# Performance work log

Hardware: AMD Instinct MI355X
Metric: run time of the kernel (lower is better)

## Reference

```python
import jax, jax.numpy as jnp
import numpy as np

B, L, D, ORDER, POS, HID, LMAX = 4, 4096, 1024, 2, 65, 64, 4096
K2 = (POS - 1) // 2

def _layernorm(x, w, b, eps=1e-5):
    m = jnp.mean(x, -1, keepdims=True)
    v = jnp.mean((x - m) ** 2, -1, keepdims=True)
    return (x - m) * jax.lax.rsqrt(v + eps) * w + b

def _fftconv(x, h, d):
    # torch: rfft(h, 2L, norm='forward') * rfft(x, 2L) -> irfft(.., norm='forward')
    # net scaling equals standard (unnormalized fwd / 1-over-n inverse) circular conv,
    # which is exactly jnp.fft default conventions.
    n = 2 * x.shape[-1]
    y = jnp.fft.irfft(jnp.fft.rfft(x, n=n) * jnp.fft.rfft(h, n=n), n=n)[..., : x.shape[-1]]
    return y + x * d

def setup_inputs() -> dict:
    key = jax.random.key(0)
    ks = jax.random.split(key, 12)
    s = 0.05
    # PositionalEncoding buffers/params (deterministic init, as in torch __init__)
    t = np.linspace(0, 1, LMAX, dtype=np.float64)[:, None]
    t_pos = np.arange(LMAX, dtype=np.float64)[:, None]
    k = np.arange(K2, dtype=np.float64)[None, :]
    z = np.exp(1j * 2 * np.pi * k * t_pos / LMAX)
    pos_z = np.concatenate([t, z.real, z.imag], axis=-1).astype(np.float32)  # (LMAX, POS)
    pos_t = t.reshape(1, 1, LMAX).astype(np.float32)
    # ExponentialDecayWindow alphas (deterministic init)
    max_decay = np.log(0.01) / 0.3
    min_decay = np.log(0.01) / 1.5
    alphas = np.linspace(min_decay, max_decay, D).reshape(1, D, 1).astype(np.float32)
    H3 = (ORDER + 1) * D
    return dict(
        u=jax.random.normal(ks[0], (B, L, D), jnp.float32),
        norm1_w=jnp.ones((D,), jnp.float32), norm1_b=jnp.zeros((D,), jnp.float32),
        proj_w=jax.random.normal(ks[1], (H3, D), jnp.float32) * s,
        proj_b=jnp.zeros((H3,), jnp.float32),
        conv_w=jax.random.normal(ks[2], (H3, 1, 3), jnp.float32) * 0.3,
        conv_b=jnp.zeros((H3,), jnp.float32),
        pos_t=jnp.asarray(pos_t), pos_z=jnp.asarray(pos_z),
        fnn_w0=jax.random.normal(ks[3], (HID, POS), jnp.float32) * s,
        fnn_b0=jnp.zeros((HID,), jnp.float32),
        freq0=8.0 * jnp.ones((1, HID), jnp.float32),
        fnn_w1=jax.random.normal(ks[4], (HID, HID), jnp.float32) * s,
        fnn_b1=jnp.zeros((HID,), jnp.float32),
        freq1=8.0 * jnp.ones((1, HID), jnp.float32),
        fnn_w2=jax.random.normal(ks[5], (HID, HID), jnp.float32) * s,
        fnn_b2=jnp.zeros((HID,), jnp.float32),
        freq2=8.0 * jnp.ones((1, HID), jnp.float32),
        fnn_wout=jax.random.normal(ks[6], (ORDER * D, HID), jnp.float32) * s,
        alphas=jnp.asarray(alphas),
        hy_bias=jax.random.normal(ks[7], (ORDER, 1, D, 1), jnp.float32),
        norm2_w=jnp.ones((D,), jnp.float32), norm2_b=jnp.zeros((D,), jnp.float32),
        fc_w=jax.random.normal(ks[8], (D, D), jnp.float32) * s,
        fc_b=jnp.zeros((D,), jnp.float32),
    )

def reference(u, norm1_w, norm1_b, proj_w, proj_b, conv_w, conv_b, pos_t, pos_z,
              fnn_w0, fnn_b0, freq0, fnn_w1, fnn_b1, freq1, fnn_w2, fnn_b2, freq2,
              fnn_wout, alphas, hy_bias, norm2_w, norm2_b, fc_w, fc_b):
    Lq = u.shape[1]
    # Projection: LN -> Linear -> depthwise short conv (causal-ish, pad=2, slice :L)
    x = _layernorm(u, norm1_w, norm1_b)
    x = jnp.einsum('bld,hd->blh', x, proj_w) + proj_b          # (B,L,3D)
    x = x.transpose(0, 2, 1)                                   # (B,3D,L)
    x = jax.lax.conv_general_dilated(
        x, conv_w, window_strides=(1,), padding=[(2, 2)],
        feature_group_count=x.shape[1],
        dimension_numbers=('NCH', 'OIH', 'NCH'))[..., :Lq] + conv_b[None, :, None]
    # HyenaFilter: sin-MLP over positional features, then exp-decay window
    zf = pos_z[:Lq]                                            # (L,POS)
    h = jnp.sin(freq0 * (zf @ fnn_w0.T + fnn_b0))
    h = jnp.sin(freq1 * (h @ fnn_w1.T + fnn_b1))
    h = jnp.sin(freq2 * (h @ fnn_w2.T + fnn_b2))
    h = (h @ fnn_wout.T).T.reshape(ORDER, D, Lq)               # (order,D,L)
    decay = jnp.exp(alphas * pos_t[..., :Lq])                  # (1,D,L)
    h = h * decay
    # order-wise gated FFT long convolution (faithful to torch chunk/broadcast semantics)
    v = x[:, -1:, :]                                           # (B,1,L)
    for i in range(ORDER):
        v = x[:, i:i + 1, :] * _fftconv(v, h[i][None], hy_bias[i])  # (B,D,L)
    y = u + v.transpose(0, 2, 1)
    out = _layernorm(y, norm2_w, norm2_b) @ fc_w.T + fc_b      # activation = identity
    return out + y
```

## Files before the change

kernel.cpp:

```cpp
#include <hip/hip_runtime.h>
#include <hip/hip_bf16.h>

#define LL 4096
#define DD 1024
#define NB 4
#define N4 4096
#define KBINS 4097
#define NSLOT4 4366
#define PI_F 3.14159265358979323846f
#define INV4 (1.0f / 4096.0f)

typedef __attribute__((ext_vector_type(4))) float f32x4;
typedef __attribute__((ext_vector_type(8))) short s16x8;

#if defined(__has_builtin)
#if __has_builtin(__builtin_amdgcn_global_load_lds)
#define USE_GLOAD_LDS 1
#endif
#endif
#ifndef USE_GLOAD_LDS
#define USE_GLOAD_LDS 0
#endif

__device__ __forceinline__ unsigned short f2bf(float f) {
  unsigned int x = __float_as_uint(f);
  x += 0x7fffu + ((x >> 16) & 1u);
  return (unsigned short)(x >> 16);
}

__device__ __forceinline__ int SLT(int n) { return n + (n >> 4) + (n >> 8); }
__device__ __forceinline__ int brev12(int n) { return (int)(__brev((unsigned)n) >> 20); }

__device__ __forceinline__ float2 cmul(float2 a, float2 b) {
  return make_float2(a.x * b.x - a.y * b.y, a.x * b.y + a.y * b.x);
}
__device__ __forceinline__ float2 cadd(float2 a, float2 b) { return make_float2(a.x + b.x, a.y + b.y); }
__device__ __forceinline__ float2 csub(float2 a, float2 b) { return make_float2(a.x - b.x, a.y - b.y); }
__device__ __forceinline__ float2 conjf(float2 a) { return make_float2(a.x, -a.y); }
__device__ __forceinline__ float2 mulni(float2 v) { return make_float2(v.y, -v.x); }
__device__ __forceinline__ float2 mulpi(float2 v) { return make_float2(-v.y, v.x); }

template<bool INV>
__device__ __forceinline__ void bfly8(float2& A0, float2& A1, float2& A2, float2& A3,
                                      float2& A4, float2& A5, float2& A6, float2& A7,
                                      float2 w1, float2 w2, float2 w3) {
  const float C8 = 0.70710678118654752f;
  float2 t;
  t = cmul(w1, A1); float2 b0 = cadd(A0, t), b1 = csub(A0, t);
  t = cmul(w1, A3); float2 b2 = cadd(A2, t), b3 = csub(A2, t);
  t = cmul(w1, A5); float2 b4 = cadd(A4, t), b5 = csub(A4, t);
  t = cmul(w1, A7); float2 b6 = cadd(A6, t), b7 = csub(A6, t);
  t = cmul(w2, b2);                     float2 c0 = cadd(b0, t), c2 = csub(b0, t);
  t = cmul(w2, b3); t = INV ? mulpi(t) : mulni(t);
  float2 c1 = cadd(b1, t), c3 = csub(b1, t);
  t = cmul(w2, b6);                     float2 c4 = cadd(b4, t), c6 = csub(b4, t);
  t = cmul(w2, b7); t = INV ? mulpi(t) : mulni(t);
  float2 c5 = cadd(b5, t), c7 = csub(b5, t);
  t = cmul(w3, c4); A0 = cadd(c0, t); A4 = csub(c0, t);
  float2 e1 = cmul(w3, c5);
  t = INV ? make_float2(C8 * (e1.x - e1.y), C8 * (e1.y + e1.x))
          : make_float2(C8 * (e1.x + e1.y), C8 * (e1.y - e1.x));
  A1 = cadd(c1, t); A5 = csub(c1, t);
  float2 e2 = cmul(w3, c6); t = INV ? mulpi(e2) : mulni(e2);
  A2 = cadd(c2, t); A6 = csub(c2, t);
  float2 e3 = cmul(w3, c7);
  t = INV ? make_float2(-C8 * (e3.x + e3.y), C8 * (e3.x - e3.y))
          : make_float2(C8 * (e3.y - e3.x), -C8 * (e3.x + e3.y));
  A3 = cadd(c3, t); A7 = csub(c3, t);
}

template<bool INV>
__device__ __forceinline__ void fft4k_01(float2* Z, const float2* __restrict__ tw) {
  const int tid = threadIdx.x;
#pragma unroll
  for (int p = 0; p < 3; ++p) {
    const int hs = 3 * p;
    const int h = 1 << hs;
    const int j0 = tid & (h - 1);
    const int i = ((tid >> hs) << (hs + 3)) + j0;
    int s0 = SLT(i),         s1 = SLT(i + h),     s2 = SLT(i + 2 * h), s3 = SLT(i + 3 * h);
    int s4 = SLT(i + 4 * h), s5 = SLT(i + 5 * h), s6 = SLT(i + 6 * h), s7 = SLT(i + 7 * h);
    float2 a0 = Z[s0], a1 = Z[s1], a2 = Z[s2], a3 = Z[s3];
    float2 a4 = Z[s4], a5 = Z[s5], a6 = Z[s6], a7 = Z[s7];
    float2 w1 = tw[j0 << (12 - hs)];
    float2 w2 = tw[j0 << (11 - hs)];
    float2 w3 = tw[j0 << (10 - hs)];
    if (INV) { w1.y = -w1.y; w2.y = -w2.y; w3.y = -w3.y; }
    bfly8<INV>(a0, a1, a2, a3, a4, a5, a6, a7, w1, w2, w3);
    Z[s0] = a0; Z[s1] = a1; Z[s2] = a2; Z[s3] = a3;
    Z[s4] = a4; Z[s5] = a5; Z[s6] = a6; Z[s7] = a7;
    __builtin_amdgcn_wave_barrier();
  }
}

template<bool INV>
__device__ __forceinline__ void fft4k_p3(const float2* Z, const float2* __restrict__ tw,
                                         float2 d[8]) {
  const int t = threadIdx.x;
#pragma unroll
  for (int k = 0; k < 8; ++k) d[k] = Z[SLT(t + 512 * k)];
  float2 w1 = tw[t << 3], w2 = tw[t << 2], w3 = tw[t << 1];
  if (INV) { w1.y = -w1.y; w2.y = -w2.y; w3.y = -w3.y; }
  bfly8<INV>(d[0], d[1], d[2], d[3], d[4], d[5], d[6], d[7], w1, w2, w3);
}

__global__ __launch_bounds__(256) void k_lnproj_ffn(
    const float* __restrict__ u, const float* __restrict__ n1w, const float* __restrict__ n1b,
    const float* __restrict__ pw, const float* __restrict__ pb,
    float* __restrict__ xp0, float* __restrict__ xp1, float* __restrict__ xpL,
    const float* __restrict__ pos_z,
    const float* __restrict__ w0, const float* __restrict__ b0, const float* __restrict__ f0,
    const float* __restrict__ w1, const float* __restrict__ b1, const float* __restrict__ f1,
    const float* __restrict__ w2, const float* __restrict__ b2, const float* __restrict__ f2,
    float* __restrict__ hid2T) {
  __shared__ float zin[4][66];
  __shared__ float hbuf[4][64];
  const int g = threadIdx.x >> 6, lane = threadIdx.x & 63;
  if (blockIdx.x < (NB * LL) / 4) {
    const int r = blockIdx.x * 4 + g;
    const float* ur = u + (size_t)r * DD;
    float4 uv[4];
    float s = 0.f, sq = 0.f;
#pragma unroll
    for (int c = 0; c < 4; ++c) {
      uv[c] = ((const float4*)ur)[lane + 64 * c];
      s += uv[c].x + uv[c].y + uv[c].z + uv[c].w;
      sq += uv[c].x * uv[c].x + uv[c].y * uv[c].y + uv[c].z * uv[c].z + uv[c].w * uv[c].w;
    }
    for (int m = 1; m < 64; m <<= 1) { s += __shfl_xor(s, m); sq += __shfl_xor(sq, m); }
    const float mean = s * (1.0f / DD);
    const float var = sq * (1.0f / DD) - mean * mean;
    const float rs = rsqrtf(var + 1e-5f);
    float d0 = 0.f, d1 = 0.f, dL = 0.f;
    const float* pwL = pw + (size_t)3071 * DD;
#pragma unroll
    for (int c = 0; c < 4; ++c) {
      int i4 = lane + 64 * c;
      float4 wv = ((const float4*)n1w)[i4];
      float4 bv = ((const float4*)n1b)[i4];
      float4 p0 = ((const float4*)pw)[i4];
      float4 p1v = ((const float4*)(pw + DD))[i4];
      float4 pLv = ((const float4*)pwL)[i4];
      float xn;
      xn = (uv[c].x - mean) * rs * wv.x + bv.x; d0 += xn * p0.x; d1 += xn * p1v.x; dL += xn * pLv.x;
      xn = (uv[c].y - mean) * rs * wv.y + bv.y; d0 += xn * p0.y; d1 += xn * p1v.y; dL += xn * pLv.y;
      xn = (uv[c].z - mean) * rs * wv.z + bv.z; d0 += xn * p0.z; d1 += xn * p1v.z; dL += xn * pLv.z;
      xn = (uv[c].w - mean) * rs * wv.w + bv.w; d0 += xn * p0.w; d1 += xn * p1v.w; dL += xn * pLv.w;
    }
    for (int m = 1; m < 64; m <<= 1) {
      d0 += __shfl_xor(d0, m); d1 += __shfl_xor(d1, m); dL += __shfl_xor(dL, m);
    }
    if (lane == 0) {
      xp0[r] = d0 + pb[0];
      xp1[r] = d1 + pb[1];
      xpL[r] = dL + pb[3071];
    }
  } else {
    const int l0 = (blockIdx.x - (NB * LL) / 4) * 16;
    for (int it = 0; it < 4; ++it) {
      const int l = l0 + g * 4 + it;
      zin[g][lane] = pos_z[(size_t)l * 65 + lane];
      if (lane == 0) zin[g][64] = pos_z[(size_t)l * 65 + 64];
      __syncthreads();
      float acc = b0[lane];
#pragma unroll
      for (int k = 0; k < 65; ++k) acc += zin[g][k] * w0[lane * 65 + k];
      float hv = sinf(f0[lane] * acc);
      __syncthreads();
      hbuf[g][lane] = hv;
      __syncthreads();
      acc = b1[lane];
#pragma unroll
      for (int k = 0; k < 64; ++k) acc += hbuf[g][k] * w1[lane * 64 + k];
      hv = sinf(f1[lane] * acc);
      __syncthreads();
      hbuf[g][lane] = hv;
      __syncthreads();
      acc = b2[lane];
#pragma unroll
      for (int k = 0; k < 64; ++k) acc += hbuf[g][k] * w2[lane * 64 + k];
      hv = sinf(f2[lane] * acc);
      hid2T[(size_t)lane * LL + l] = hv;
      __syncthreads();
    }
  }
}

__global__ __launch_bounds__(256) void k_tapconv_prep(
    const float* __restrict__ xp0, const float* __restrict__ xp1, const float* __restrict__ xpL,
    const float* __restrict__ cw, const float* __restrict__ cb,
    float* __restrict__ x0c, float* __restrict__ x1c, float* __restrict__ xLc,
    float2* tw, const float* __restrict__ fcw, unsigned short* __restrict__ fcwb) {
  const int bid = blockIdx.x;
  if (bid < 64) {
    int idx = bid * 256 + threadIdx.x;
    int l = idx & (LL - 1);
    int base = idx - l;
    {
      const float* a = xp0 + base;
      float v = cw[2] * a[l];
      if (l >= 1) v += cw[1] * a[l - 1];
      if (l >= 2) v += cw[0] * a[l - 2];
      x0c[idx] = v + cb[0];
    }
    {
      const float* a = xp1 + base;
      float v = cw[5] * a[l];
      if (l >= 1) v += cw[4] * a[l - 1];
      if (l >= 2) v += cw[3] * a[l - 2];
      x1c[idx] = v + cb[1];
    }
    {
      const float* a = xpL + base;
      float v = cw[3071 * 3 + 2] * a[l];
      if (l >= 1) v += cw[3071 * 3 + 1] * a[l - 1];
      if (l >= 2) v += cw[3071 * 3 + 0] * a[l - 2];
      xLc[idx] = v + cb[3071];
    }
  } else if (bid < 80) {
    int k = (bid - 64) * 256 + threadIdx.x;
    float ang = -2.0f * PI_F * (float)k / 8192.0f;
    float s, c;
    sincosf(ang, &s, &c);
    tw[k] = make_float2(c, s);
  } else {
    int i = (bid - 80) * 256 + threadIdx.x;
    float4 v = ((const float4*)fcw)[i];
    ushort4 o;
    o.x = f2bf(v.x); o.y = f2bf(v.y); o.z = f2bf(v.z); o.w = f2bf(v.w);
    ((ushort4*)fcwb)[i] = o;
  }
}

#define FG_CH 16
__global__ __launch_bounds__(256) void k_filter_gemm(
    const float* __restrict__ hid2T, const float* __restrict__ wout,
    const float* __restrict__ alphas, const float* __restrict__ pos_t,
    float* __restrict__ h) {
  __shared__ float wdl[FG_CH][64];
  const int cg = blockIdx.x & 127;
  const int lg = blockIdx.x >> 7;
  const int t = threadIdx.x;
  for (int idx = t; idx < FG_CH * 64; idx += 256) {
    int c = idx >> 6, k = idx & 63;
    wdl[c][k] = wout[(size_t)(cg * FG_CH + c) * 64 + k];
  }
  __syncthreads();
  const int l0 = lg * 1024 + 4 * t;
  float4 acc[FG_CH];
#pragma unroll
  for (int c = 0; c < FG_CH; ++c) acc[c] = make_float4(0.f, 0.f, 0.f, 0.f);
  for (int k = 0; k < 64; ++k) {
    float4 hv = *(const float4*)&hid2T[(size_t)k * LL + l0];
#pragma unroll
    for (int c = 0; c < FG_CH; ++c) {
      acc[c].x = fmaf(hv.x, wdl[c][k], acc[c].x);
      acc[c].y = fmaf(hv.y, wdl[c][k], acc[c].y);
      acc[c].z = fmaf(hv.z, wdl[c][k], acc[c].z);
      acc[c].w = fmaf(hv.w, wdl[c][k], acc[c].w);
    }
  }
  float4 tt = *(const float4*)&pos_t[l0];
#pragma unroll
  for (int c = 0; c < FG_CH; ++c) {
    int ch = cg * FG_CH + c;
    float a = alphas[ch & (DD - 1)];
    float4 o;
    o.x = acc[c].x * expf(a * tt.x);
    o.y = acc[c].y * expf(a * tt.y);
    o.z = acc[c].z * expf(a * tt.z);
    o.w = acc[c].w * expf(a * tt.w);
    *(float4*)&h[(size_t)ch * LL + l0] = o;
  }
}

__global__ __launch_bounds__(512, 4) void k_fft_filters(
    const float* __restrict__ h, const float* __restrict__ xLc,
    float2* __restrict__ Hs, float2* __restrict__ V0s, const float2* __restrict__ tw) {
  __shared__ float2 Z[NSLOT4];
  const int tid = threadIdx.x;
  const int bid = blockIdx.x;
  const float2* src = (bid < 2048) ? (const float2*)(h + (size_t)bid * LL)
                                   : (const float2*)(xLc + (size_t)(bid - 2048) * LL);
  float2* Out = (bid < 2048) ? (Hs + (size_t)bid * KBINS)
                             : (V0s + (size_t)(bid - 2048) * KBINS);
#pragma unroll
  for (int gi = 0; gi < 4; ++gi) {
    int j = tid + gi * 512;
    float2 v = src[j];
    int r = brev12(j);
    Z[SLT(r)] = v;
    Z[SLT(r + 1)] = make_float2(0.f, 0.f);
  }
  __syncthreads();
  fft4k_01<false>(Z, tw);
  __syncthreads();
  float2 dd[8];
  fft4k_p3<false>(Z, tw, dd);
#pragma unroll
  for (int k = 0; k < 8; ++k) Z[SLT(tid + 512 * k)] = dd[k];
  __syncthreads();
#pragma unroll
  for (int gi = 0; gi < 4; ++gi) {
    int k = tid + gi * 512;
    float2 zk = Z[SLT(k)];
    float2 zm = Z[SLT((N4 - k) & (N4 - 1))];
    float2 B = conjf(zm);
    float2 E = make_float2(0.5f * (zk.x + B.x), 0.5f * (zk.y + B.y));
    float2 F = make_float2(0.5f * (zk.x - B.x), 0.5f * (zk.y - B.y));
    float2 G = cmul(tw[k], F);
    float2 WO = mulni(G);
    Out[k] = cadd(E, WO);
    Out[N4 - k] = conjf(csub(E, WO));
  }
  if (tid == 0) {
    float2 zc = Z[SLT(2048)];
    float2 F = make_float2(0.f, zc.y);
    float2 G = cmul(tw[2048], F);
    Out[2048] = cadd(make_float2(zc.x, 0.f), mulni(G));
  }
}

__global__ __launch_bounds__(512, 4) void k_conv12(
    const float2* __restrict__ Hs, const float2* __restrict__ V0s,
    const float* __restrict__ x0c, const float* __restrict__ x1c, const float* __restrict__ xLc,
    const float* __restrict__ hyb, float* __restrict__ v2, const float2* __restrict__ tw) {
  __shared__ float2 Z[NSLOT4];
  const int b = blockIdx.x >> 10, d = blockIdx.x & 1023;
  const int tid = threadIdx.x;
  const float2* H0 = Hs + (size_t)d * KBINS;
  const float2* H1 = Hs + (size_t)(DD + d) * KBINS;
  const float2* V = V0s + (size_t)b * KBINS;
  const float2* g0 = (const float2*)(x0c + (size_t)b * LL);
  const float2* g1 = (const float2*)(x1c + (size_t)b * LL);
  const float2* v0 = (const float2*)(xLc + (size_t)b * LL);
  float2 gg0[4], vv0[4];
#pragma unroll
  for (int k = 0; k < 4; ++k) {
    int j = tid + 512 * k;
    gg0[k] = g0[j];
    vv0[k] = v0[j];
  }
#pragma unroll
  for (int gi = 0; gi < 4; ++gi) {
    int k = tid + gi * 512;
    int m = N4 - k;
    float2 Yk = cmul(V[k], H0[k]);
    float2 Ym = cmul(V[m], H0[m]);
    float2 B = conjf(Ym);
    float2 E = make_float2(0.5f * (Yk.x + B.x), 0.5f * (Yk.y + B.y));
    float2 F = make_float2(0.5f * (Yk.x - B.x), 0.5f * (Yk.y - B.y));
    float2 O = cmul(conjf(tw[k]), F);
    float2 iO = mulpi(O);
    Z[SLT(brev12(k))] = cadd(E, iO);
    if (k > 0) Z[SLT(brev12(m))] = conjf(csub(E, iO));
  }
  if (tid == 0) {
    float2 A = cmul(V[2048], H0[2048]);
    float2 F = make_float2(0.f, A.y);
    float2 O = cmul(conjf(tw[2048]), F);
    Z[SLT(brev12(2048))] = cadd(make_float2(A.x, 0.f), mulpi(O));
  }
  __syncthreads();
  fft4k_01<true>(Z, tw);
  __syncthreads();
  float2 dA[8];
  fft4k_p3<true>(Z, tw, dA);
  const float bd0 = hyb[d], bd1 = hyb[DD + d];
  float2 vsave[4];
#pragma unroll
  for (int k = 0; k < 4; ++k) {
    vsave[k] = make_float2(gg0[k].x * fmaf(dA[k].x, INV4, bd0 * vv0[k].x),
                           gg0[k].y * fmaf(dA[k].y, INV4, bd0 * vv0[k].y));
  }
  __syncthreads();
#pragma unroll
  for (int k = 0; k < 4; ++k) {
    int j = tid + 512 * k;
    int r = brev12(j);
    Z[SLT(r)] = vsave[k];
    Z[SLT(r + 1)] = make_float2(0.f, 0.f);
  }
  __syncthreads();
  fft4k_01<false>(Z, tw);
  __syncthreads();
  float2 dB[8];
  fft4k_p3<false>(Z, tw, dB);
#pragma unroll
  for (int k = 0; k < 8; ++k) Z[SLT(tid + 512 * k)] = dB[k];
  __syncthreads();
  float2 gg1[4];
#pragma unroll
  for (int k = 0; k < 4; ++k) gg1[k] = g1[tid + 512 * k];
  float2 zpk[4], zpm[4], z2048;
#pragma unroll
  for (int gi = 0; gi < 4; ++gi) {
    int k = tid + gi * 512;
    int m = N4 - k;
    float2 zk = Z[SLT(k)];
    float2 zm = Z[SLT(m & (N4 - 1))];
    float2 B = conjf(zm);
    float2 E = make_float2(0.5f * (zk.x + B.x), 0.5f * (zk.y + B.y));
    float2 F = make_float2(0.5f * (zk.x - B.x), 0.5f * (zk.y - B.y));
    float2 wk = tw[k];
    float2 G = cmul(wk, F);
    float2 WO = mulni(G);
    float2 Xk = cadd(E, WO);
    float2 Xm = conjf(csub(E, WO));
    float2 Yk = cmul(Xk, H1[k]);
    float2 Ym = cmul(Xm, H1[m]);
    float2 B2 = conjf(Ym);
    float2 E2 = make_float2(0.5f * (Yk.x + B2.x), 0.5f * (Yk.y + B2.y));
    float2 F2 = make_float2(0.5f * (Yk.x - B2.x), 0.5f * (Yk.y - B2.y));
    float2 O2 = cmul(conjf(wk), F2);
    float2 iO2 = mulpi(O2);
    zpk[gi] = cadd(E2, iO2);
    zpm[gi] = conjf(csub(E2, iO2));
  }
  if (tid == 0) {
    float2 zc = Z[SLT(2048)];
    float2 F = make_float2(0.f, zc.y);
    float2 G = cmul(tw[2048], F);
    float2 Xk = cadd(make_float2(zc.x, 0.f), mulni(G));
    float2 Y = cmul(Xk, H1[2048]);
    float2 F2 = make_float2(0.f, Y.y);
    float2 O2 = cmul(conjf(tw[2048]), F2);
    z2048 = cadd(make_float2(Y.x, 0.f), mulpi(O2));
  }
  __syncthreads();
#pragma unroll
  for (int gi = 0; gi < 4; ++gi) {
    int k = tid + gi * 512;
    Z[SLT(brev12(k))] = zpk[gi];
    if (k > 0) Z[SLT(brev12(N4 - k))] = zpm[gi];
  }
  if (tid == 0) Z[SLT(brev12(2048))] = z2048;
  __syncthreads();
  fft4k_01<true>(Z, tw);
  __syncthreads();
  float2 dC[8];
  fft4k_p3<true>(Z, tw, dC);
  float2* out2 = (float2*)(v2 + ((size_t)b * DD + d) * LL);
#pragma unroll
  for (int k = 0; k < 4; ++k) {
    int j = tid + 512 * k;
    out2[j] = make_float2(gg1[k].x * fmaf(dC[k].x, INV4, bd1 * vsave[k].x),
                          gg1[k].y * fmaf(dC[k].y, INV4, bd1 * vsave[k].y));
  }
}

__global__ __launch_bounds__(256) void k_transpose_add(const float* __restrict__ v2,
                                                       const float* __restrict__ u,
                                                       float* __restrict__ y) {
  __shared__ float T[64][65];
  const int bid = blockIdx.x;
  const int lt = bid & 63, dt = (bid >> 6) & 15, b = bid >> 10;
  const int t = threadIdx.x;
  const int tdr = t >> 2, lc0 = (t & 3) * 16;
  const float* vp = v2 + ((size_t)(b * DD + dt * 64 + tdr)) * LL + lt * 64 + lc0;
#pragma unroll
  for (int q = 0; q < 4; ++q) {
    float4 vv = ((const float4*)vp)[q];
    T[tdr][lc0 + 4 * q + 0] = vv.x;
    T[tdr][lc0 + 4 * q + 1] = vv.y;
    T[tdr][lc0 + 4 * q + 2] = vv.z;
    T[tdr][lc0 + 4 * q + 3] = vv.w;
  }
  __syncthreads();
  const int dc = t & 63, lg = t >> 6;
#pragma unroll
  for (int lr0 = 0; lr0 < 64; lr0 += 4) {
    int lr = lr0 + lg;
    size_t idx = ((size_t)b * LL + lt * 64 + lr) * DD + dt * 64 + dc;
    y[idx] = u[idx] + T[dc][lr];
  }
}

__global__ __launch_bounds__(256) void k_ln2(const float* __restrict__ y,
                                             const float* __restrict__ w,
                                             const float* __restrict__ bb,
                                             unsigned short* __restrict__ yln) {
  const int wid = threadIdx.x >> 6, lane = threadIdx.x & 63;
  const size_t r = (size_t)blockIdx.x * 4 + wid;
  const float* yr = y + r * DD;
  float4 v[4];
  float s = 0.f, sq = 0.f;
#pragma unroll
  for (int c = 0; c < 4; ++c) {
    v[c] = ((const float4*)yr)[lane + 64 * c];
    s += v[c].x + v[c].y + v[c].z + v[c].w;
    sq += v[c].x * v[c].x + v[c].y * v[c].y + v[c].z * v[c].z + v[c].w * v[c].w;
  }
  for (int m = 1; m < 64; m <<= 1) { s += __shfl_xor(s, m); sq += __shfl_xor(sq, m); }
  const float mean = s * (1.0f / DD);
  const float var = sq * (1.0f / DD) - mean * mean;
  const float rs = rsqrtf(var + 1e-5f);
#pragma unroll
  for (int c = 0; c < 4; ++c) {
    int i4 = lane + 64 * c;
    float4 wv = ((const float4*)w)[i4];
    float4 bv = ((const float4*)bb)[i4];
    ushort4 o;
    o.x = f2bf((v[c].x - mean) * rs * wv.x + bv.x);
    o.y = f2bf((v[c].y - mean) * rs * wv.y + bv.y);
    o.z = f2bf((v[c].z - mean) * rs * wv.z + bv.z);
    o.w = f2bf((v[c].w - mean) * rs * wv.w + bv.w);
    ((ushort4*)(yln + r * DD))[i4] = o;
  }
}

#define GBM 128
#define GBN 128
#define GBK 64
#if USE_GLOAD_LDS
#define LDK 64
#else
#define LDK 72
#endif

__global__ __launch_bounds__(256) void k_gemm(const short* __restrict__ A,
                                              const short* __restrict__ Bw,
                                              const float* __restrict__ fcb,
                                              const float* __restrict__ yy,
                                              float* __restrict__ out) {
  __shared__ short As[GBM * LDK];
  __shared__ short Bs[GBN * LDK];
  const int t = threadIdx.x;
  const int bm = blockIdx.x & 127;
  const int bn = blockIdx.x >> 7;
  const int wave = t >> 6, lane = t & 63;
  const int wr = wave >> 1, wc = wave & 1;
  const int rrow = lane & 15, kb = (lane >> 4) * 8;

  f32x4 acc[4][4];
#pragma unroll
  for (int i = 0; i < 4; ++i)
#pragma unroll
    for (int j = 0; j < 4; ++j) acc[i][j] = (f32x4){0.f, 0.f, 0.f, 0.f};

  const size_t abase = (size_t)(bm * GBM) * 1024;
  const size_t bbase = (size_t)(bn * GBN) * 1024;

  for (int k0 = 0; k0 < 1024; k0 += GBK) {
#if USE_GLOAD_LDS
    {
      const int r0 = wave * 32;
      const int lrow = lane >> 3, loff = (lane & 7) * 8;
#pragma unroll
      for (int q = 0; q < 4; ++q) {
        const int row = r0 + 8 * q + lrow;
        __builtin_amdgcn_global_load_lds(
            (const __attribute__((address_space(1))) void*)(A + abase + (size_t)row * 1024 + k0 + loff),
            (__attribute__((address_space(3))) void*)&As[(r0 + 8 * q) * LDK], 16, 0, 0);
        __builtin_amdgcn_global_load_lds(
            (const __attribute__((address_space(1))) void*)(Bw + bbase + (size_t)row * 1024 + k0 + loff),
            (__attribute__((address_space(3))) void*)&Bs[(r0 + 8 * q) * LDK], 16, 0, 0);
      }
    }
#else
#pragma unroll
    for (int c = 0; c < 4; ++c) {
      int chunk = c * 256 + t;
      int row = chunk >> 3, off = (chunk & 7) * 8;
      s16x8 av = *(const s16x8*)(A + abase + (size_t)row * 1024 + k0 + off);
      *(s16x8*)&As[row * LDK + off] = av;
      s16x8 bv = *(const s16x8*)(Bw + bbase + (size_t)row * 1024 + k0 + off);
      *(s16x8*)&Bs[row * LDK + off] = bv;
    }
#endif
    __syncthreads();
    s16x8 af[2][4], bfr[2][4];
#pragma unroll
    for (int ks = 0; ks < 2; ++ks) {
#pragma unroll
      for (int mr = 0; mr < 4; ++mr)
        af[ks][mr] = *(const s16x8*)&As[(wr * 64 + mr * 16 + rrow) * LDK + ks * 32 + kb];
#pragma unroll
      for (int nc = 0; nc < 4; ++nc)
        bfr[ks][nc] = *(const s16x8*)&Bs[(wc * 64 + nc * 16 + rrow) * LDK + ks * 32 + kb];
    }
#pragma unroll
    for (int ks = 0; ks < 2; ++ks)
#pragma unroll
      for (int mr = 0; mr < 4; ++mr)
#pragma unroll
        for (int nc = 0; nc < 4; ++nc)
          acc[mr][nc] = __builtin_amdgcn_mfma_f32_16x16x32_bf16(af[ks][mr], bfr[ks][nc],
                                                                acc[mr][nc], 0, 0, 0);
    __syncthreads();
  }
  const int cg = lane >> 4, cr = lane & 15;
#pragma unroll
  for (int mr = 0; mr < 4; ++mr)
#pragma unroll
    for (int nc = 0; nc < 4; ++nc) {
      f32x4 a = acc[mr][nc];
      int col = bn * GBN + wc * 64 + nc * 16 + cr;
#pragma unroll
      for (int q = 0; q < 4; ++q) {
        int row = bm * GBM + wr * 64 + mr * 16 + cg * 4 + q;
        size_t idx = (size_t)row * 1024 + col;
        out[idx] = a[q] + fcb[col] + yy[idx];
      }
    }
}

extern "C" void kernel_launch(void* const* d_in, const int* in_sizes, int n_in,
                              void* d_out, int out_size, void* d_ws, size_t ws_size,
                              hipStream_t stream) {
  const float* u      = (const float*)d_in[0];
  const float* n1w    = (const float*)d_in[1];
  const float* n1b    = (const float*)d_in[2];
  const float* projw  = (const float*)d_in[3];
  const float* projb  = (const float*)d_in[4];
  const float* convw  = (const float*)d_in[5];
  const float* convb  = (const float*)d_in[6];
  const float* pos_t  = (const float*)d_in[7];
  const float* pos_z  = (const float*)d_in[8];
  const float* w0     = (const float*)d_in[9];
  const float* b0     = (const float*)d_in[10];
  const float* f0     = (const float*)d_in[11];
  const float* w1     = (const float*)d_in[12];
  const float* b1     = (const float*)d_in[13];
  const float* f1     = (const float*)d_in[14];
  const float* w2     = (const float*)d_in[15];
  const float* b2     = (const float*)d_in[16];
  const float* f2     = (const float*)d_in[17];
  const float* wout   = (const float*)d_in[18];
  const float* alphas = (const float*)d_in[19];
  const float* hyb    = (const float*)d_in[20];
  const float* n2w    = (const float*)d_in[21];
  const float* n2b    = (const float*)d_in[22];
  const float* fcw    = (const float*)d_in[23];
  const float* fcb    = (const float*)d_in[24];

  char* wsb = (char*)d_ws;
  size_t off = 0;
  auto alloc = [&](size_t bytes) -> void* {
    off = (off + 255) & ~(size_t)255;
    void* p = wsb + off;
    off += bytes;
    return p;
  };
  float2* tw    = (float2*)alloc(sizeof(float2) * 4096);
  float*  xp0   = (float*)alloc(sizeof(float) * NB * LL);
  float*  xp1   = (float*)alloc(sizeof(float) * NB * LL);
  float*  xpL   = (float*)alloc(sizeof(float) * NB * LL);
  float*  x0c   = (float*)alloc(sizeof(float) * NB * LL);
  float*  x1c   = (float*)alloc(sizeof(float) * NB * LL);
  float*  xLc   = (float*)alloc(sizeof(float) * NB * LL);
  float*  hid2T = (float*)alloc(sizeof(float) * 64 * LL);
  float2* Hs    = (float2*)alloc(sizeof(float2) * 2 * DD * KBINS);
  float2* V0s   = (float2*)alloc(sizeof(float2) * NB * KBINS);
  float*  v2    = (float*)alloc(sizeof(float) * NB * DD * LL);
  unsigned short* fcwb = (unsigned short*)alloc(sizeof(unsigned short) * DD * DD);
  float*          y   = (float*)Hs;
  unsigned short* yln = (unsigned short*)v2;
  float*          h   = v2;
  (void)ws_size; (void)in_sizes; (void)n_in; (void)out_size;

  k_lnproj_ffn<<<(NB * LL) / 4 + LL / 16, 256, 0, stream>>>(
      u, n1w, n1b, projw, projb, xp0, xp1, xpL,
      pos_z, w0, b0, f0, w1, b1, f1, w2, b2, f2, hid2T);
  k_tapconv_prep<<<64 + 16 + (DD * DD / 4) / 256, 256, 0, stream>>>(
      xp0, xp1, xpL, convw, convb, x0c, x1c, xLc, tw, fcw, fcwb);
  k_filter_gemm<<<512, 256, 0, stream>>>(hid2T, wout, alphas, pos_t, h);
  k_fft_filters<<<2048 + NB, 512, 0, stream>>>(h, xLc, Hs, V0s, tw);
  k_conv12<<<NB * DD, 512, 0, stream>>>(Hs, V0s, x0c, x1c, xLc, hyb, v2, tw);
  k_transpose_add<<<4096, 256, 0, stream>>>(v2, u, y);
  k_ln2<<<(NB * LL) / 4, 256, 0, stream>>>(y, n2w, n2b, yln);
  k_gemm<<<(16384 / GBM) * (1024 / GBN), 256, 0, stream>>>((const short*)yln, (const short*)fcwb,
                                                           fcb, y, (float*)d_out);
}
```

Baseline: 362.3 us.

## Fuse transpose-add with LayerNorm2 and accumulate GEMM residual in place

Merges the transpose-plus-residual kernel and the second LayerNorm into one kernel that stages a 16-row tile of all 1024 channels in shared memory, adds u, computes row statistics, and writes both y and its bf16 normalized copy. This removes the round trip of re-reading y from global memory and one kernel launch. y now lives in the output buffer and the GEMM epilogue adds into out in place, so a separate y workspace is no longer read. The column-strided LDS writes in the transpose may cause bank conflicts, and fewer, larger blocks change occupancy.

```diff
diff --git a/kernel.cpp b/kernel.cpp
--- a/kernel.cpp
+++ b/kernel.cpp
@@ -449,63 +449,66 @@
   }
 }
 
-__global__ __launch_bounds__(256) void k_transpose_add(const float* __restrict__ v2,
-                                                       const float* __restrict__ u,
-                                                       float* __restrict__ y) {
-  __shared__ float T[64][65];
-  const int bid = blockIdx.x;
-  const int lt = bid & 63, dt = (bid >> 6) & 15, b = bid >> 10;
+#define TL 16
+__global__ __launch_bounds__(512) void k_transpose_ln2(
+    const float* __restrict__ v2, const float* __restrict__ u,
+    const float* __restrict__ w, const float* __restrict__ bb,
+    float* __restrict__ y, unsigned short* __restrict__ yln) {
+  __shared__ float T[TL][1028];
+  const int b = blockIdx.x >> 8;
+  const int lb = (blockIdx.x & 255) * TL;
   const int t = threadIdx.x;
-  const int tdr = t >> 2, lc0 = (t & 3) * 16;
-  const float* vp = v2 + ((size_t)(b * DD + dt * 64 + tdr)) * LL + lt * 64 + lc0;
-#pragma unroll
-  for (int q = 0; q < 4; ++q) {
-    float4 vv = ((const float4*)vp)[q];
-    T[tdr][lc0 + 4 * q + 0] = vv.x;
-    T[tdr][lc0 + 4 * q + 1] = vv.y;
-    T[tdr][lc0 + 4 * q + 2] = vv.z;
-    T[tdr][lc0 + 4 * q + 3] = vv.w;
-  }
-  __syncthreads();
-  const int dc = t & 63, lg = t >> 6;
-#pragma unroll
-  for (int lr0 = 0; lr0 < 64; lr0 += 4) {
-    int lr = lr0 + lg;
-    size_t idx = ((size_t)b * LL + lt * 64 + lr) * DD + dt * 64 + dc;
-    y[idx] = u[idx] + T[dc][lr];
-  }
-}
-
-__global__ __launch_bounds__(256) void k_ln2(const float* __restrict__ y,
-                                             const float* __restrict__ w,
-                                             const float* __restrict__ bb,
-                                             unsigned short* __restrict__ yln) {
-  const int wid = threadIdx.x >> 6, lane = threadIdx.x & 63;
-  const size_t r = (size_t)blockIdx.x * 4 + wid;
-  const float* yr = y + r * DD;
-  float4 v[4];
-  float s = 0.f, sq = 0.f;
-#pragma unroll
-  for (int c = 0; c < 4; ++c) {
-    v[c] = ((const float4*)yr)[lane + 64 * c];
-    s += v[c].x + v[c].y + v[c].z + v[c].w;
-    sq += v[c].x * v[c].x + v[c].y * v[c].y + v[c].z * v[c].z + v[c].w * v[c].w;
-  }
-  for (int m = 1; m < 64; m <<= 1) { s += __shfl_xor(s, m); sq += __shfl_xor(sq, m); }
-  const float mean = s * (1.0f / DD);
-  const float var = sq * (1.0f / DD) - mean * mean;
-  const float rs = rsqrtf(var + 1e-5f);
-#pragma unroll
-  for (int c = 0; c < 4; ++c) {
-    int i4 = lane + 64 * c;
-    float4 wv = ((const float4*)w)[i4];
-    float4 bv = ((const float4*)bb)[i4];
-    ushort4 o;
-    o.x = f2bf((v[c].x - mean) * rs * wv.x + bv.x);
-    o.y = f2bf((v[c].y - mean) * rs * wv.y + bv.y);
-    o.z = f2bf((v[c].z - mean) * rs * wv.z + bv.z);
-    o.w = f2bf((v[c].w - mean) * rs * wv.w + bv.w);
-    ((ushort4*)(yln + r * DD))[i4] = o;
+#pragma unroll
+  for (int dd = 0; dd < 2; ++dd) {
+    const int d = t + dd * 512;
+    const float4* src = (const float4*)(v2 + ((size_t)b * DD + d) * LL + lb);
+#pragma unroll
+    for (int q = 0; q < 4; ++q) {
+      float4 v = src[q];
+      T[4 * q + 0][d] = v.x;
+      T[4 * q + 1][d] = v.y;
+      T[4 * q + 2][d] = v.z;
+      T[4 * q + 3][d] = v.w;
+    }
+  }
+  __syncthreads();
+  const int wv = t >> 6, lane = t & 63;
+#pragma unroll
+  for (int rr = 0; rr < 2; ++rr) {
+    const int row = wv * 2 + rr;
+    const int l = lb + row;
+    const float* urow = u + ((size_t)b * LL + l) * DD;
+    float4 v[4];
+    float s = 0.f, sq = 0.f;
+#pragma unroll
+    for (int c = 0; c < 4; ++c) {
+      int i4 = lane + 64 * c;
+      float4 tv = *(const float4*)&T[row][4 * i4];
+      float4 uv = ((const float4*)urow)[i4];
+      tv.x += uv.x; tv.y += uv.y; tv.z += uv.z; tv.w += uv.w;
+      v[c] = tv;
+      s += tv.x + tv.y + tv.z + tv.w;
+      sq += tv.x * tv.x + tv.y * tv.y + tv.z * tv.z + tv.w * tv.w;
+    }
+    for (int m = 1; m < 64; m <<= 1) { s += __shfl_xor(s, m); sq += __shfl_xor(sq, m); }
+    const float mean = s * (1.0f / DD);
+    const float var = sq * (1.0f / DD) - mean * mean;
+    const float rs = rsqrtf(var + 1e-5f);
+    float* yrow = y + ((size_t)b * LL + l) * DD;
+    unsigned short* ybr = yln + ((size_t)b * LL + l) * DD;
+#pragma unroll
+    for (int c = 0; c < 4; ++c) {
+      int i4 = lane + 64 * c;
+      float4 wv4 = ((const float4*)w)[i4];
+      float4 bv = ((const float4*)bb)[i4];
+      ((float4*)yrow)[i4] = v[c];
+      ushort4 o;
+      o.x = f2bf((v[c].x - mean) * rs * wv4.x + bv.x);
+      o.y = f2bf((v[c].y - mean) * rs * wv4.y + bv.y);
+      o.z = f2bf((v[c].z - mean) * rs * wv4.z + bv.z);
+      o.w = f2bf((v[c].w - mean) * rs * wv4.w + bv.w);
+      ((ushort4*)ybr)[i4] = o;
+    }
   }
 }
 
@@ -521,8 +524,7 @@
 __global__ __launch_bounds__(256) void k_gemm(const short* __restrict__ A,
                                               const short* __restrict__ Bw,
                                               const float* __restrict__ fcb,
-                                              const float* __restrict__ yy,
-                                              float* __restrict__ out) {
+                                              float* out) {
   __shared__ short As[GBM * LDK];
   __shared__ short Bs[GBN * LDK];
   const int t = threadIdx.x;
@@ -600,7 +602,7 @@
       for (int q = 0; q < 4; ++q) {
         int row = bm * GBM + wr * 64 + mr * 16 + cg * 4 + q;
         size_t idx = (size_t)row * 1024 + col;
-        out[idx] = a[q] + fcb[col] + yy[idx];
+        out[idx] = a[q] + fcb[col] + out[idx];
       }
     }
 }
@@ -654,8 +656,8 @@
   float2* V0s   = (float2*)alloc(sizeof(float2) * NB * KBINS);
   float*  v2    = (float*)alloc(sizeof(float) * NB * DD * LL);
   unsigned short* fcwb = (unsigned short*)alloc(sizeof(unsigned short) * DD * DD);
-  float*          y   = (float*)Hs;
-  unsigned short* yln = (unsigned short*)v2;
+  float*          y   = (float*)d_out;
+  unsigned short* yln = (unsigned short*)Hs;
   float*          h   = v2;
   (void)ws_size; (void)in_sizes; (void)n_in; (void)out_size;
 
@@ -667,8 +669,7 @@
   k_filter_gemm<<<512, 256, 0, stream>>>(hid2T, wout, alphas, pos_t, h);
   k_fft_filters<<<2048 + NB, 512, 0, stream>>>(h, xLc, Hs, V0s, tw);
   k_conv12<<<NB * DD, 512, 0, stream>>>(Hs, V0s, x0c, x1c, xLc, hyb, v2, tw);
-  k_transpose_add<<<4096, 256, 0, stream>>>(v2, u, y);
-  k_ln2<<<(NB * LL) / 4, 256, 0, stream>>>(y, n2w, n2b, yln);
+  k_transpose_ln2<<<NB * (LL / TL), 512, 0, stream>>>(v2, u, n2w, n2b, y, yln);
   k_gemm<<<(16384 / GBM) * (1024 / GBN), 256, 0, stream>>>((const short*)yln, (const short*)fcwb,
-                                                           fcb, y, (float*)d_out);
-}
+                                                           fcb, (float*)d_out);
+}
```

Measured after the change: 368.8 us. Within noise of the previous version (+1.8%).
